# Kernel tuning notes

Measured on AMD Instinct MI355X. Metric: run time of the kernel, lower is better.

## Reference

```python
import jax, jax.numpy as jnp
import numpy as np

DIM = 192; HEADS = 6; WIN = 8; HIDDEN = int(DIM * 2.66); EPS = 1e-5

def dct_matrix(n):
    # DCT-II orthonormal matrix, matches get_dctMatrix(n, n)
    i = np.arange(n)[:, None]; j = np.arange(n)[None, :]
    M = np.cos(np.pi * i * (2 * j + 1) / (2 * n)) * np.sqrt(2.0 / n)
    M[0, :] = np.sqrt(1.0 / n)
    return jnp.asarray(M, dtype=jnp.float32)

def layernorm_c(x, w, b):
    # WithBias LayerNorm over channel dim of BCHW (restormer to_3d/to_4d style)
    mu = x.mean(axis=1, keepdims=True)
    var = ((x - mu) ** 2).mean(axis=1, keepdims=True)
    return (x - mu) / jnp.sqrt(var + EPS) * w[None, :, None, None] + b[None, :, None, None]

def conv1x1(x, w, b=None):
    y = jnp.einsum('oc,bchw->bohw', w, x)
    return y if b is None else y + b[None, :, None, None]

def dwconv3x3(x, w):
    return jax.lax.conv_general_dilated(x, w, (1, 1), ((1, 1), (1, 1)),
        dimension_numbers=('NCHW', 'OIHW', 'NCHW'), feature_group_count=x.shape[1])

def l2norm(x):
    n = jnp.sqrt(jnp.sum(x * x, axis=-1, keepdims=True))
    return x / jnp.maximum(n, 1e-12)

def window_channel_attn(qkv, temperature):
    # 'b (z head c) (h1 h) (w1 w) -> z (b h1 w1) head c (h w)'
    b, _, H, W = qkv.shape
    cph = DIM // HEADS
    h1, w1 = H // WIN, W // WIN
    t = qkv.reshape(b, 3, HEADS, cph, h1, WIN, w1, WIN)
    t = t.transpose(1, 0, 4, 6, 2, 3, 5, 7).reshape(3, b * h1 * w1, HEADS, cph, WIN * WIN)
    q, k, v = t[0], t[1], t[2]
    q = l2norm(q); k = l2norm(k)
    attn = jnp.einsum('nhce,nhde->nhcd', q, k) * temperature[None]  # channel x channel per window
    attn = jax.nn.softmax(attn, axis=-1)
    out = jnp.einsum('nhcd,nhde->nhce', attn, v)
    out = out.reshape(b, h1, w1, HEADS, cph, WIN, WIN)
    out = out.transpose(0, 3, 4, 1, 5, 2, 6).reshape(b, DIM, H, W)
    return out

def forward(x, norm1_w, norm1_b, w_qkv, w_dw, temperature, w_proj, b_proj,
            norm2_w, norm2_b, w_in, w_dwf, w_out):
    B, C, H, W = x.shape
    Mh = dct_matrix(H); Mw = dct_matrix(W)
    # attention branch in DCT domain
    y = layernorm_c(x, norm1_w, norm1_b)
    y = jnp.einsum('ph,bchw->bcpw', Mh, y)      # dct2dx: Mh @ y @ Mw.T
    y = jnp.einsum('bcpw,qw->bcpq', y, Mw)
    qkv = dwconv3x3(conv1x1(y, w_qkv), w_dw)
    a = window_channel_attn(qkv, temperature)
    a = conv1x1(a, w_proj, b_proj)
    a = jnp.einsum('bcpq,qw->bcpw', a, Mw)      # idct2dx: Mh.T @ a @ Mw
    a = jnp.einsum('bcpw,ph->bchw', a, Mh)
    x1 = x + a
    # gated-dconv FFN branch
    z = layernorm_c(x1, norm2_w, norm2_b)
    f = dwconv3x3(conv1x1(z, w_in), w_dwf)
    f1, f2 = jnp.split(f, 2, axis=1)
    f = jax.nn.gelu(f1, approximate=False) * f2
    f = conv1x1(f, w_out)
    return x1 + f

def setup_inputs() -> dict:
    key = jax.random.key(0)
    ks = jax.random.split(key, 8)
    B, C, H, W = 2, DIM, 192, 192
    s = 0.02
    return {
        'x': jax.random.normal(ks[0], (B, C, H, W), jnp.float32),
        'norm1_w': jnp.ones((C,), jnp.float32),
        'norm1_b': jnp.zeros((C,), jnp.float32),
        'w_qkv': jax.random.normal(ks[1], (3 * C, C), jnp.float32) * s,
        'w_dw': jax.random.normal(ks[2], (3 * C, 1, 3, 3), jnp.float32) * s,
        'temperature': jnp.ones((HEADS, 1, 1), jnp.float32) / np.float32(np.sqrt(C)),
        'w_proj': jax.random.normal(ks[3], (C, C), jnp.float32) * s,
        'b_proj': jnp.zeros((C,), jnp.float32),
        'norm2_w': jnp.ones((C,), jnp.float32),
        'norm2_b': jnp.zeros((C,), jnp.float32),
        'w_in': jax.random.normal(ks[4], (2 * HIDDEN, C), jnp.float32) * s,
        'w_dwf': jax.random.normal(ks[5], (2 * HIDDEN, 1, 3, 3), jnp.float32) * s,
        'w_out': jax.random.normal(ks[6], (C, HIDDEN), jnp.float32) * s,
    }

def reference(x, norm1_w, norm1_b, w_qkv, w_dw, temperature, w_proj, b_proj,
              norm2_w, norm2_b, w_in, w_dwf, w_out):
    return forward(x, norm1_w, norm1_b, w_qkv, w_dw, temperature, w_proj, b_proj,
                   norm2_w, norm2_b, w_in, w_dwf, w_out)
```

## Files before the change

### kernel.cpp

```cpp
#include <hip/hip_runtime.h>
#include <hip/hip_bf16.h>

typedef __hip_bfloat16 bft;
typedef __attribute__((ext_vector_type(8))) short bf16x8;
typedef __attribute__((ext_vector_type(4))) float f32x4;

#define BLK 256
static constexpr int Cc = 192;
static constexpr int L  = 192;
static constexpr int S  = 36864;
static constexpr int Bn = 2;
static constexpr int HID = 510;
static constexpr int CH2 = 96;
static constexpr int FTR2 = (CH2 + 2) * L;
static constexpr int GTR2 = CH2 * L;
static constexpr int DWS = 225;
static constexpr double PI_D = 3.141592653589793238462643383279502884;

__device__ __forceinline__ float ldf(const float* p) { return *p; }
__device__ __forceinline__ float ldf(const bft* p)   { return __bfloat162float(*p); }
__device__ __forceinline__ void  stf(float* p, float v) { *p = v; }
__device__ __forceinline__ void  stf(bft* p, float v)   { *p = __float2bfloat16(v); }
__device__ __forceinline__ unsigned short f2bfu(float f) {
    bft h = __float2bfloat16(f);
    return *reinterpret_cast<const unsigned short*>(&h);
}
__device__ __forceinline__ float bu2f(unsigned short u) {
    unsigned int x = (unsigned int)u << 16;
    return __uint_as_float(x);
}
__device__ __forceinline__ bf16x8 ld8(const unsigned short* p) {
    union { unsigned int u[4]; bf16x8 v; } t;
    const unsigned int* q = reinterpret_cast<const unsigned int*>(p);
    t.u[0] = q[0]; t.u[1] = q[1]; t.u[2] = q[2]; t.u[3] = q[3];
    return t.v;
}
__device__ __forceinline__ void softbar() {
    asm volatile("s_waitcnt lgkmcnt(0)" ::: "memory");
    __builtin_amdgcn_sched_barrier(0);
    __builtin_amdgcn_s_barrier();
}

__global__ __launch_bounds__(BLK) void k_dct_init(bft* __restrict__ dctb,
                                                  bft* __restrict__ dctTb) {
    int idx = blockIdx.x * BLK + threadIdx.x;
    if (idx >= L * L) return;
    int p = idx / L, h = idx - p * L;
    double v = (p == 0) ? sqrt(1.0 / L)
                        : cos(PI_D * p * (2 * h + 1) / (2.0 * L)) * sqrt(2.0 / L);
    bft bv = __float2bfloat16((float)v);
    dctb[p * L + h] = bv;
    dctTb[h * L + p] = bv;
}

__global__ __launch_bounds__(BLK) void k_cvt(const float* __restrict__ src,
                                             bft* __restrict__ dst,
                                             int Mr, int Kr, int Kp) {
    int idx = blockIdx.x * BLK + threadIdx.x;
    int m = idx / Kp, k = idx - m * Kp;
    float v = (m < Mr && k < Kr) ? src[(size_t)m * Kr + k] : 0.f;
    dst[idx] = __float2bfloat16(v);
}

__global__ __launch_bounds__(BLK) void k_cvt_ffn(const float* __restrict__ src,
                                                 bft* __restrict__ dst) {
    int idx = blockIdx.x * BLK + threadIdx.x;
    int m = idx / Cc, k = idx - m * Cc;
    float v = 0.f;
    if (m < 510) v = src[(size_t)m * Cc + k];
    else if (m >= 512 && m < 1022) v = src[(size_t)(m - 2) * Cc + k];
    dst[idx] = __float2bfloat16(v);
}

template <typename TI, bool TRANS>
__global__ __launch_bounds__(BLK) void k_lnt(const TI* __restrict__ x,
                                             const float* __restrict__ w,
                                             const float* __restrict__ b,
                                             bft* __restrict__ out,
                                             long zI, long zO) {
    __shared__ float t[192][65];
    __shared__ float mus[64], rs[64];
    const int tid = threadIdx.x;
    const int s0 = blockIdx.x * 64;
    const TI* xp = x + (size_t)blockIdx.y * zI;
    if constexpr (sizeof(TI) == 4) {
        for (int id = tid; id < 192 * 16; id += BLK) {
            int c = id >> 4, q = id & 15;
            float4 v = *reinterpret_cast<const float4*>(
                (const float*)xp + (size_t)c * S + s0 + q * 4);
            t[c][q * 4 + 0] = v.x; t[c][q * 4 + 1] = v.y;
            t[c][q * 4 + 2] = v.z; t[c][q * 4 + 3] = v.w;
        }
    } else {
        for (int id = tid; id < 192 * 8; id += BLK) {
            int c = id >> 3, q = id & 7;
            uint4 raw = *reinterpret_cast<const uint4*>(
                (const bft*)xp + (size_t)c * S + s0 + q * 8);
            const unsigned short* u = reinterpret_cast<const unsigned short*>(&raw);
#pragma unroll
            for (int e = 0; e < 8; ++e) t[c][q * 8 + e] = bu2f(u[e]);
        }
    }
    __syncthreads();
    {
        int px = tid >> 2, g = tid & 3;
        float sum = 0.f, sq = 0.f;
#pragma unroll
        for (int j = 0; j < 48; ++j) {
            float v = t[g * 48 + j][px];
            sum += v; sq += v * v;
        }
        sum += __shfl_xor(sum, 1); sum += __shfl_xor(sum, 2);
        sq  += __shfl_xor(sq, 1);  sq  += __shfl_xor(sq, 2);
        float mu = sum * (1.f / Cc);
        float var = sq * (1.f / Cc) - mu * mu;
        float r = rsqrtf(var + 1e-5f);
        if (g == 0) { mus[px] = mu; rs[px] = r; }
    }
    __syncthreads();
    bft* op = out + (size_t)blockIdx.y * zO;
    if constexpr (!TRANS) {
        for (int id = tid; id < 192 * 8; id += BLK) {
            int c = id >> 3, q = id & 7;
            float wc = w[c], bc = b[c];
            unsigned short v8[8];
#pragma unroll
            for (int e = 0; e < 8; ++e) {
                int px = q * 8 + e;
                v8[e] = f2bfu((t[c][px] - mus[px]) * rs[px] * wc + bc);
            }
            *reinterpret_cast<uint4*>(op + (size_t)c * S + s0 + q * 8) =
                *reinterpret_cast<uint4*>(v8);
        }
    } else {
#pragma unroll
        for (int qq = 0; qq < 3; ++qq) {
            for (int id = tid; id < 512; id += BLK) {
                int s = id >> 3, qlo = id & 7;
                int q = qq * 8 + qlo;
                float mu = mus[s], r = rs[s];
                unsigned short v8[8];
#pragma unroll
                for (int e = 0; e < 8; ++e) {
                    int c = q * 8 + e;
                    v8[e] = f2bfu((t[c][s] - mu) * r * w[c] + b[c]);
                }
                *reinterpret_cast<uint4*>(op + (size_t)(s0 + s) * Cc + q * 8) =
                    *reinterpret_cast<uint4*>(v8);
            }
        }
    }
}

__global__ __launch_bounds__(BLK) void k_tr(const bft* __restrict__ in,
                                            bft* __restrict__ out, long z) {
    __shared__ unsigned short t[32][72];
    const int tid = threadIdx.x;
    const int s0 = blockIdx.x * 64, c0 = blockIdx.y * 32;
    const bft* ip = in + (size_t)blockIdx.z * z;
    bft* op = out + (size_t)blockIdx.z * z;
    {
        int c = tid >> 3, sc = (tid & 7) * 8;
        *reinterpret_cast<uint4*>(&t[c][sc]) =
            *reinterpret_cast<const uint4*>(ip + (size_t)(c0 + c) * S + s0 + sc);
    }
    __syncthreads();
    {
        int s = tid >> 2, cc = (tid & 3) * 8;
        unsigned short v[8];
#pragma unroll
        for (int q = 0; q < 8; ++q) v[q] = t[cc + q][s];
        *reinterpret_cast<uint4*>(op + (size_t)(s0 + s) * Cc + c0 + cc) =
            *reinterpret_cast<uint4*>(v);
    }
}

__global__ __launch_bounds__(BLK) void k_w2s(const bft* __restrict__ src,
                                             bft* __restrict__ dst,
                                             long zI, long zO) {
    __shared__ unsigned short t[192][100];
    const int tid = threadIdx.x;
    const int hh = blockIdx.x;
    const int ch0 = blockIdx.y * 96;
    const int bz = blockIdx.z;
    const int h1 = hh >> 3, ii = hh & 7;
    const bft* ip = src + (size_t)bz * zI;
    for (int id = tid; id < 192 * 12; id += BLK) {
        int r = id / 12, q = id - r * 12;
        int w1 = r >> 3, jj = r & 7;
        int s = (h1 * 24 + w1) * 64 + ii * 8 + jj;
        *reinterpret_cast<uint4*>(&t[r][q * 8]) =
            *reinterpret_cast<const uint4*>(ip + (size_t)s * Cc + ch0 + q * 8);
    }
    __syncthreads();
    bft* op = dst + (size_t)bz * zO;
    for (int id = tid; id < 96 * 24; id += BLK) {
        int c = id / 24, q = id - c * 24;
        unsigned short v[8];
#pragma unroll
        for (int e = 0; e < 8; ++e) v[e] = t[q * 8 + e][c];
        *reinterpret_cast<uint4*>(op + (size_t)(ch0 + c) * S + (size_t)hh * L + q * 8) =
            *reinterpret_cast<uint4*>(v);
    }
}

template <int WR, int WC, int FM, int FN, int KSTEP, int BMODE, int OMODE,
          bool GSWAP, bool SWIZ, bool AMASK, bool HASBIAS, bool BIASN,
          bool HASRES, typename OutT, typename ResT>
__global__ __launch_bounds__(256) void k_mm(
    const bft* __restrict__ A, int strideA, int Mreal, long zA,
    const bft* __restrict__ B, int strideB, long zB,
    OutT* __restrict__ Out, int strideO, long zO,
    const float* __restrict__ bias,
    const ResT* __restrict__ Res, long zR,
    int K, int rlo, int rhi) {
    static_assert(WR == 2 && WC == 2, "split epilogues assume 2x2 waves");
    constexpr int BM = WR * FM * 16, BN = WC * FN * 16;
    constexpr int AV = KSTEP / 8;
    constexpr int KL = (BM + BN) * (KSTEP + 8);
    constexpr int RSTH = (OMODE == 3) ? (BN / 2) * (BM + 8)
                       : (OMODE == 5 ? (BM / 2) * (BN + 8) : 0);
    constexpr int LDSZ = (KL > RSTH) ? KL : RSTH;
    __shared__ unsigned short lds[LDSZ];
    unsigned short (*Al)[KSTEP + 8] =
        reinterpret_cast<unsigned short(*)[KSTEP + 8]>(lds);
    unsigned short (*Bl)[KSTEP + 8] =
        reinterpret_cast<unsigned short(*)[KSTEP + 8]>(lds + BM * (KSTEP + 8));
    const int tid = threadIdx.x;
    int bx = blockIdx.x, by = blockIdx.y;
    if constexpr (SWIZ) {
        int nbx = gridDim.x, nby = gridDim.y;
        int nwg = nbx * nby;
        int orig = bx + nbx * by;
        int cpx = nwg >> 3;
        int swz = (orig & 7) * cpx + (orig >> 3);
        bx = swz % nbx; by = swz / nbx;
    }
    const int n0 = (GSWAP ? by : bx) * BN;
    const int m0 = (GSWAP ? bx : by) * BM;
    const int bz = blockIdx.z;
    const int lane = tid & 63, wv = tid >> 6;
    const int wr = wv / WC, wc = wv % WC;
    const int l15 = lane & 15, l4 = lane >> 4;
    f32x4 acc[FM][FN] = {};

    const bft* Ab = A + (size_t)bz * zA;
    const bft* Bb = B + (size_t)bz * zB;

    for (int k0 = 0; k0 < K; k0 += KSTEP) {
        for (int id = tid; id < BM * AV; id += 256) {
            int row = id / AV, kc = (id % AV) * 8;
            int gm = m0 + row;
            if constexpr (AMASK) {
                uint4 val = make_uint4(0, 0, 0, 0);
                if (gm >= rlo && gm < rhi)
                    val = *reinterpret_cast<const uint4*>(
                        Ab + (size_t)gm * strideA + k0 + kc);
                *reinterpret_cast<uint4*>(&Al[row][kc]) = val;
            } else {
                if (gm >= Mreal) gm = Mreal - 1;
                *reinterpret_cast<uint4*>(&Al[row][kc]) =
                    *reinterpret_cast<const uint4*>(Ab + (size_t)gm * strideA + k0 + kc);
            }
        }
        for (int id = tid; id < BN * AV; id += 256) {
            int row = id / AV, kc = (id % AV) * 8;
            int gn = n0 + row;
            uint4 val;
            if constexpr (BMODE == 2) {
                val = *reinterpret_cast<const uint4*>(
                    Bb + (size_t)gn * strideB + k0 + kc);
            } else {
                if (gn >= rlo && gn < rhi)
                    val = *reinterpret_cast<const uint4*>(
                        Bb + (size_t)gn * strideB + k0 + kc);
                else
                    val = make_uint4(0, 0, 0, 0);
            }
            *reinterpret_cast<uint4*>(&Bl[row][kc]) = val;
        }
        __syncthreads();
#pragma unroll
        for (int kk = 0; kk < KSTEP / 32; ++kk) {
            bf16x8 af[FM], bf[FN];
#pragma unroll
            for (int i = 0; i < FM; ++i)
                af[i] = *reinterpret_cast<const bf16x8*>(
                    &Al[wr * FM * 16 + i * 16 + l15][kk * 32 + l4 * 8]);
#pragma unroll
            for (int j = 0; j < FN; ++j)
                bf[j] = *reinterpret_cast<const bf16x8*>(
                    &Bl[wc * FN * 16 + j * 16 + l15][kk * 32 + l4 * 8]);
#pragma unroll
            for (int i = 0; i < FM; ++i)
#pragma unroll
                for (int j = 0; j < FN; ++j)
                    acc[i][j] = __builtin_amdgcn_mfma_f32_16x16x32_bf16(
                        af[i], bf[j], acc[i][j], 0, 0, 0);
        }
        __syncthreads();
    }
    if constexpr (OMODE == 3) {
        constexpr int OST = BM + 8;
        constexpr int HBN = BN / 2;
        unsigned short* Ol = lds;
        constexpr int TPR = BM / 64;
#pragma unroll
        for (int h = 0; h < 2; ++h) {
            if (wc == h) {
#pragma unroll
                for (int i = 0; i < FM; ++i) {
                    int mB = wr * FM * 16 + i * 16 + l4 * 4;
#pragma unroll
                    for (int j = 0; j < FN; ++j) {
                        int nl = j * 16 + l15;
                        unsigned short v[4];
#pragma unroll
                        for (int r = 0; r < 4; ++r) v[r] = f2bfu(acc[i][j][r]);
                        *reinterpret_cast<uint2*>(&Ol[nl * OST + mB]) =
                            *reinterpret_cast<uint2*>(v);
                    }
                }
            }
            softbar();
            for (int row = tid / TPR; row < HBN; row += 256 / TPR) {
                int seg = (tid % TPR) * 64;
                bft* dst = (bft*)Out + (size_t)bz * zO
                         + (size_t)(n0 + h * HBN + row) * strideO + m0 + seg;
                const unsigned short* src = &Ol[row * OST + seg];
#pragma unroll
                for (int q = 0; q < 8; ++q)
                    *reinterpret_cast<uint4*>(dst + q * 8) =
                        *reinterpret_cast<const uint4*>(src + q * 8);
            }
            if (h == 0) softbar();
        }
        return;
    }
    if constexpr (OMODE == 5) {
        constexpr int OST = BN + 8;
        constexpr int HBM = BM / 2;
        unsigned short* Ol = lds;
        constexpr int TPR = BN / 64;
#pragma unroll
        for (int h = 0; h < 2; ++h) {
            if (wr == h) {
#pragma unroll
                for (int i = 0; i < FM; ++i) {
                    int mBl = i * 16 + l4 * 4;
#pragma unroll
                    for (int j = 0; j < FN; ++j) {
                        int n = wc * FN * 16 + j * 16 + l15;
                        float bn = 0.f;
                        if constexpr (HASBIAS && BIASN) bn = bias[n0 + n];
#pragma unroll
                        for (int r = 0; r < 4; ++r)
                            Ol[(mBl + r) * OST + n] = f2bfu(acc[i][j][r] + bn);
                    }
                }
            }
            softbar();
            for (int row = tid / TPR; row < HBM; row += 256 / TPR) {
                int m = m0 + h * HBM + row;
                if (m >= Mreal) continue;
                int seg = (tid % TPR) * 64;
                bft* dst = (bft*)Out + (size_t)bz * zO
                         + (size_t)m * strideO + n0 + seg;
                const unsigned short* src = &Ol[row * OST + seg];
                if constexpr (HASRES) {
                    const ResT* res = Res + (size_t)bz * zR
                                    + (size_t)m * strideO + n0 + seg;
#pragma unroll
                    for (int q = 0; q < 8; ++q) {
                        uint4 lv = *reinterpret_cast<const uint4*>(src + q * 8);
                        const unsigned short* le =
                            reinterpret_cast<const unsigned short*>(&lv);
                        unsigned short ov[8];
#pragma unroll
                        for (int e = 0; e < 8; ++e)
                            ov[e] = f2bfu(bu2f(le[e]) + ldf(res + q * 8 + e));
                        *reinterpret_cast<uint4*>(dst + q * 8) =
                            *reinterpret_cast<uint4*>(ov);
                    }
                } else {
#pragma unroll
                    for (int q = 0; q < 8; ++q)
                        *reinterpret_cast<uint4*>(dst + q * 8) =
                            *reinterpret_cast<const uint4*>(src + q * 8);
                }
            }
            if (h == 0) softbar();
        }
        return;
    }
#pragma unroll
    for (int i = 0; i < FM; ++i) {
        int mB = m0 + wr * FM * 16 + i * 16 + l4 * 4;
#pragma unroll
        for (int j = 0; j < FN; ++j) {
            int n = n0 + wc * FN * 16 + j * 16 + l15;
#pragma unroll
            for (int r = 0; r < 4; ++r) {
                int m = mB + r;
                if (m >= Mreal) continue;
                float vv = acc[i][j][r];
                if constexpr (HASBIAS) vv += BIASN ? bias[n] : bias[m];
                size_t idx = (size_t)bz * zO + (size_t)m * strideO + n;
                if constexpr (HASRES)
                    vv += ldf(Res + (size_t)bz * zR + (size_t)m * strideO + n);
                stf(Out + idx, vv);
            }
        }
    }
}

__global__ __launch_bounds__(BLK) void k_dwconv3b(const bft* __restrict__ qkv,
                                                  const float* __restrict__ wt,
                                                  bft* __restrict__ q_out,
                                                  bft* __restrict__ k_out,
                                                  bft* __restrict__ v_out,
                                                  long CSl) {
    __shared__ float t[10 * DWS];
    const int tid = threadIdx.x;
    const int ch3 = blockIdx.x;
    const int wr = blockIdx.y;
    const int b = ch3 / 576, zc = ch3 - b * 576;
    const int z = zc / Cc, ch = zc - z * Cc;
    const int h0 = wr * 8;
    const bft* ip = qkv + (size_t)b * 3 * CSl + (size_t)zc * S;
    for (int id = tid; id < 240; id += BLK) {
        int row = id / 24, q = id - row * 24;
        int gh = h0 - 1 + row;
        float e[8];
        if (gh >= 0 && gh < L) {
            uint4 raw = *reinterpret_cast<const uint4*>(ip + (size_t)gh * L + q * 8);
            const unsigned short* u = reinterpret_cast<const unsigned short*>(&raw);
#pragma unroll
            for (int ee = 0; ee < 8; ++ee) e[ee] = bu2f(u[ee]);
        } else {
#pragma unroll
            for (int ee = 0; ee < 8; ++ee) e[ee] = 0.f;
        }
#pragma unroll
        for (int ee = 0; ee < 8; ++ee) t[row * DWS + 1 + q * 8 + ee] = e[ee];
    }
    if (tid < 10) { t[tid * DWS] = 0.f; t[tid * DWS + 193] = 0.f; }
    __syncthreads();
    if (tid >= 192) return;
    float wv9[9];
#pragma unroll
    for (int i = 0; i < 9; ++i) wv9[i] = wt[(size_t)zc * 9 + i];
    const int wl = tid >> 3;
    const int ii = tid & 7;
    const int w0 = wl * 8;
    float acc[8] = {};
#pragma unroll
    for (int dy = 0; dy < 3; ++dy) {
        const float* rowp = &t[(ii + dy) * DWS + w0];
#pragma unroll
        for (int dx = 0; dx < 3; ++dx) {
            float wgt = wv9[dy * 3 + dx];
#pragma unroll
            for (int jj = 0; jj < 8; ++jj)
                acc[jj] += wgt * rowp[jj + dx];
        }
    }
    bft* base = (z == 0) ? q_out : (z == 1) ? k_out : v_out;
    unsigned short ov[8];
#pragma unroll
    for (int jj = 0; jj < 8; ++jj) ov[jj] = f2bfu(acc[jj]);
    *reinterpret_cast<uint4*>(base + (size_t)b * CSl + (size_t)ch * S
                              + (size_t)(wr * 24 + wl) * 64 + ii * 8) =
        *reinterpret_cast<uint4*>(ov);
}

__global__ __launch_bounds__(256) void k_attn_mfma(
    const bft* __restrict__ QW, long zQ,
    const bft* __restrict__ KW, long zK,
    const bft* __restrict__ VW, long zV,
    const float* __restrict__ temp,
    bft* __restrict__ outp, long zO) {
    __shared__ unsigned short qls[4][32 * 66];
    __shared__ unsigned short kls[4][32 * 66];
    __shared__ unsigned short vls[4][32 * 66];
    __shared__ float rqs[4][32], rks[4][32];
    const int tid = threadIdx.x;
    const int wv = tid >> 6, lane = tid & 63;
    const int win = blockIdx.x * 4 + wv;
    const int hd = blockIdx.y;
    const int bz = blockIdx.z;
    const int l15 = lane & 15, l4 = lane >> 4;
    unsigned short* ql = qls[wv];
    unsigned short* kl = kls[wv];
    unsigned short* vl = vls[wv];
    const size_t base = (size_t)(hd * 32) * S + (size_t)win * 64;

#pragma unroll
    for (int i = 0; i < 4; ++i) {
        int c = i * 8 + (lane >> 3), e0 = (lane & 7) * 8;
        size_t g = base + (size_t)c * S + e0;
        uint4 vq = *reinterpret_cast<const uint4*>(QW + (size_t)bz * zQ + g);
        uint4 vk = *reinterpret_cast<const uint4*>(KW + (size_t)bz * zK + g);
        uint4 vvv = *reinterpret_cast<const uint4*>(VW + (size_t)bz * zV + g);
        unsigned int* dq = reinterpret_cast<unsigned int*>(&ql[c * 66 + e0]);
        unsigned int* dk = reinterpret_cast<unsigned int*>(&kl[c * 66 + e0]);
        unsigned int* dv = reinterpret_cast<unsigned int*>(&vl[c * 66 + e0]);
        dq[0] = vq.x; dq[1] = vq.y; dq[2] = vq.z; dq[3] = vq.w;
        dk[0] = vk.x; dk[1] = vk.y; dk[2] = vk.z; dk[3] = vk.w;
        dv[0] = vvv.x; dv[1] = vvv.y; dv[2] = vvv.z; dv[3] = vvv.w;
    }
    __syncthreads();
    {
        int row = lane & 31;
        const unsigned short* src = (lane < 32) ? ql : kl;
        float s = 0.f;
#pragma unroll
        for (int w = 0; w < 32; ++w) {
            unsigned int d = *reinterpret_cast<const unsigned int*>(&src[row * 66 + 2 * w]);
            float a = bu2f((unsigned short)(d & 0xffff));
            float b = bu2f((unsigned short)(d >> 16));
            s += a * a + b * b;
        }
        float r = 1.f / fmaxf(sqrtf(s), 1e-12f);
        if (lane < 32) rqs[wv][row] = r; else rks[wv][row] = r;
    }
    __syncthreads();
    f32x4 at[2][2] = {};
#pragma unroll
    for (int ks = 0; ks < 2; ++ks) {
        bf16x8 aq[2], bk[2];
#pragma unroll
        for (int i = 0; i < 2; ++i)
            aq[i] = ld8(&ql[(i * 16 + l15) * 66 + ks * 32 + l4 * 8]);
#pragma unroll
        for (int j = 0; j < 2; ++j)
            bk[j] = ld8(&kl[(j * 16 + l15) * 66 + ks * 32 + l4 * 8]);
#pragma unroll
        for (int i = 0; i < 2; ++i)
#pragma unroll
            for (int j = 0; j < 2; ++j)
                at[i][j] = __builtin_amdgcn_mfma_f32_16x16x32_bf16(
                    aq[i], bk[j], at[i][j], 0, 0, 0);
    }
    float tpr = temp[hd];
    float rk0 = rks[wv][l15] * tpr, rk1 = rks[wv][16 + l15] * tpr;
    float pr[2][2][4];
#pragma unroll
    for (int i = 0; i < 2; ++i)
#pragma unroll
        for (int r = 0; r < 4; ++r) {
            int c = i * 16 + l4 * 4 + r;
            float rq = rqs[wv][c];
            float v0 = at[i][0][r] * rq * rk0;
            float v1 = at[i][1][r] * rq * rk1;
            float mx = fmaxf(v0, v1);
#pragma unroll
            for (int m = 1; m < 16; m <<= 1) mx = fmaxf(mx, __shfl_xor(mx, m));
            v0 = __expf(v0 - mx);
            v1 = __expf(v1 - mx);
            float sm = v0 + v1;
#pragma unroll
            for (int m = 1; m < 16; m <<= 1) sm += __shfl_xor(sm, m);
            float inv = 1.f / sm;
            pr[i][0][r] = v0 * inv;
            pr[i][1][r] = v1 * inv;
        }
    __syncthreads();
    unsigned short* pl = ql;
#pragma unroll
    for (int i = 0; i < 2; ++i)
#pragma unroll
        for (int j = 0; j < 2; ++j)
#pragma unroll
            for (int r = 0; r < 4; ++r)
                pl[(i * 16 + l4 * 4 + r) * 34 + j * 16 + l15] = f2bfu(pr[i][j][r]);
    __syncthreads();
    bf16x8 ap[2];
#pragma unroll
    for (int i = 0; i < 2; ++i)
        ap[i] = ld8(&pl[(i * 16 + l15) * 34 + l4 * 8]);
    f32x4 o[2][4] = {};
#pragma unroll
    for (int j = 0; j < 4; ++j) {
        unsigned short tv[8];
#pragma unroll
        for (int q = 0; q < 8; ++q)
            tv[q] = vl[(l4 * 8 + q) * 66 + j * 16 + l15];
        bf16x8 bv = *reinterpret_cast<bf16x8*>(tv);
#pragma unroll
        for (int i = 0; i < 2; ++i)
            o[i][j] = __builtin_amdgcn_mfma_f32_16x16x32_bf16(ap[i], bv, o[i][j], 0, 0, 0);
    }
#pragma unroll
    for (int i = 0; i < 2; ++i)
#pragma unroll
        for (int j = 0; j < 4; ++j) {
            int e = j * 16 + l15, cl = i * 16 + l4 * 4;
            unsigned short v[4];
#pragma unroll
            for (int r = 0; r < 4; ++r) v[r] = f2bfu(o[i][j][r]);
            unsigned short* row = ((e < 32) ? kl : vl) + (e & 31) * 40 + cl;
            *reinterpret_cast<uint2*>(row) = *reinterpret_cast<uint2*>(v);
        }
    {
        const unsigned short* row = ((lane < 32) ? kl : vl) + (lane & 31) * 40;
        bft* dst = outp + (size_t)bz * zO + (size_t)(win * 64 + lane) * Cc + hd * 32;
#pragma unroll
        for (int q = 0; q < 4; ++q)
            *reinterpret_cast<uint4*>(dst + q * 8) =
                *reinterpret_cast<const uint4*>(row + q * 8);
    }
}

__global__ __launch_bounds__(BLK) void k_gateT(const bft* __restrict__ fTg,
                                               const float* __restrict__ wt,
                                               bft* __restrict__ gTg) {
    __shared__ float w1s[64][9];
    __shared__ float w2s[64][9];
    const int tid = threadIdx.x;
    const int cbase = blockIdx.y * 64;
    const bft* fT = fTg + (size_t)blockIdx.z * FTR2 * 1024;
    bft* gT = gTg + (size_t)blockIdx.z * GTR2 * 512;
    for (int id = tid; id < 576; id += BLK) {
        int cl = id / 9, k = id - cl * 9;
        int c = cbase + cl;
        w1s[cl][k] = (c < HID) ? wt[(size_t)c * 9 + k] : 0.f;
        w2s[cl][k] = (c < HID) ? wt[(size_t)(c + HID) * 9 + k] : 0.f;
    }
    __syncthreads();
    int px = blockIdx.x * 32 + (tid >> 3);
    int cgl = (tid & 7) * 8;
    int hc = px / L, w = px - hc * L;
    float a1[8] = {}, a2[8] = {};
#pragma unroll
    for (int dy = 0; dy < 3; ++dy) {
#pragma unroll
        for (int dx = 0; dx < 3; ++dx) {
            int ww = w + dx - 1;
            if (ww < 0 || ww >= L) continue;
            size_t frow = (size_t)((hc + dy) * L + ww) * 1024 + cbase + cgl;
            uint4 u1 = *reinterpret_cast<const uint4*>(fT + frow);
            uint4 u2 = *reinterpret_cast<const uint4*>(fT + frow + 512);
            const unsigned short* e1 = reinterpret_cast<const unsigned short*>(&u1);
            const unsigned short* e2 = reinterpret_cast<const unsigned short*>(&u2);
            int k = dy * 3 + dx;
#pragma unroll
            for (int j = 0; j < 8; ++j) {
                a1[j] += w1s[cgl + j][k] * bu2f(e1[j]);
                a2[j] += w2s[cgl + j][k] * bu2f(e2[j]);
            }
        }
    }
    unsigned short ov[8];
#pragma unroll
    for (int j = 0; j < 8; ++j) {
        float ge = 0.5f * a1[j] * (1.f + erff(a1[j] * 0.70710678118654752f));
        ov[j] = f2bfu(ge * a2[j]);
    }
    *reinterpret_cast<uint4*>(gT + (size_t)px * 512 + cbase + cgl) =
        *reinterpret_cast<uint4*>(ov);
}

extern "C" void kernel_launch(void* const* d_in, const int* in_sizes, int n_in,
                              void* d_out, int out_size, void* d_ws, size_t ws_size,
                              hipStream_t stream) {
    const float* x      = (const float*)d_in[0];
    const float* n1w    = (const float*)d_in[1];
    const float* n1b    = (const float*)d_in[2];
    const float* w_qkv  = (const float*)d_in[3];
    const float* w_dw   = (const float*)d_in[4];
    const float* temp   = (const float*)d_in[5];
    const float* w_proj = (const float*)d_in[6];
    const float* b_proj = (const float*)d_in[7];
    const float* n2w    = (const float*)d_in[8];
    const float* n2b    = (const float*)d_in[9];
    const float* w_in   = (const float*)d_in[10];
    const float* w_dwf  = (const float*)d_in[11];
    const float* w_out  = (const float*)d_in[12];
    float* outp = (float*)d_out;

    const long CS = (long)Cc * S;
    const size_t DCT_B = 147456;
    const size_t BUF_B = (size_t)Bn * CS * 2;
    const size_t QKV_B = (size_t)Bn * 3 * CS * 2;
    const size_t WB_B  = 884736;
    const size_t GT_B  = (size_t)Bn * GTR2 * 512 * 2;
    const size_t NEED  = DCT_B + 4 * BUF_B + QKV_B + WB_B + GT_B;
    if (ws_size < NEED) return;

    char* p = (char*)d_ws;
    bft* dctb  = (bft*)p;
    bft* dctTb = dctb + L * L;
    p += DCT_B;
    bft* X1    = (bft*)p;                  p += BUF_B;
    bft* PbB   = (bft*)p;                  p += BUF_B;
    bft* QbB   = (bft*)p;                  p += BUF_B;
    bft* VW    = (bft*)p;                  p += BUF_B;
    bft* QKV   = (bft*)p;                  p += QKV_B;
    bft* w_qkv_b = (bft*)p;
    bft* w_proj_b = w_qkv_b + 576 * 192;
    bft* w_in_b  = w_proj_b + 192 * 192;
    bft* w_out_b = w_in_b + 1024 * 192;
    p += WB_B;
    bft* gT = (bft*)p;
    bft* fT = QKV;
    bft* attnT = QKV + CS;

    k_dct_init<<<144, BLK, 0, stream>>>(dctb, dctTb);
    k_cvt<<<432, BLK, 0, stream>>>(w_qkv, w_qkv_b, 576, 192, 192);
    k_cvt<<<144, BLK, 0, stream>>>(w_proj, w_proj_b, 192, 192, 192);
    k_cvt_ffn<<<768, BLK, 0, stream>>>(w_in, w_in_b);
    k_cvt<<<384, BLK, 0, stream>>>(w_out, w_out_b, 192, 510, 512);

    k_lnt<float, false><<<dim3(S / 64, Bn), BLK, 0, stream>>>(x, n1w, n1b, PbB, CS, CS);
    k_mm<2, 2, 2, 6, 32, 2, 3, false, false, false, false, false, false, bft, float><<<dim3(1, 3, Bn * Cc), 256, 0, stream>>>(
        PbB, L, L, S,  dctb, L, 0,  QbB, L, S,  nullptr, nullptr, 0,  L, 0, 0);
    k_mm<2, 2, 2, 6, 32, 2, 3, false, false, false, false, false, false, bft, float><<<dim3(1, 3, Bn * Cc), 256, 0, stream>>>(
        QbB, L, L, S,  dctb, L, 0,  PbB, L, S,  nullptr, nullptr, 0,  L, 0, 0);
    k_tr<<<dim3(576, 6, Bn), BLK, 0, stream>>>(PbB, QbB, CS);
    k_mm<2, 2, 4, 4, 32, 2, 5, true, true, false, false, false, false, bft, float><<<dim3(5, 288, Bn), 256, 0, stream>>>(
        w_qkv_b, Cc, 576, 0,  QbB, Cc, CS,  QKV, S, 3 * CS,  nullptr, nullptr, 0,  Cc, 0, 0);
    k_dwconv3b<<<dim3(Bn * 576, 24), BLK, 0, stream>>>(QKV, w_dw, PbB, QbB, VW, CS);
    k_attn_mfma<<<dim3(144, 6, Bn), 256, 0, stream>>>(
        PbB, CS, QbB, CS, VW, CS, temp, attnT, 3 * CS);
    k_mm<2, 2, 2, 6, 32, 2, 5, false, false, false, true, true, false, bft, float><<<dim3(1, 576, Bn), 256, 0, stream>>>(
        attnT, Cc, S, 3 * CS,  w_proj_b, Cc, 0,  PbB, Cc, CS,  b_proj, (const float*)nullptr, 0,  Cc, 0, 0);
    k_w2s<<<dim3(192, 2, Bn), BLK, 0, stream>>>(PbB, QbB, CS, CS);
    k_mm<2, 2, 2, 6, 32, 2, 3, false, false, false, false, false, false, bft, float><<<dim3(1, 3, Bn * Cc), 256, 0, stream>>>(
        QbB, L, L, S,  dctTb, L, 0,  PbB, L, S,  nullptr, nullptr, 0,  L, 0, 0);
    k_mm<2, 2, 2, 6, 32, 2, 5, false, false, false, false, false, true, bft, float><<<dim3(1, 3, Bn * Cc), 256, 0, stream>>>(
        dctTb, L, L, 0,  PbB, L, S,  X1, L, S,  nullptr, x, S,  L, 0, 0);

    k_lnt<bft, true><<<dim3(S / 64, Bn), BLK, 0, stream>>>(X1, n2w, n2b, QbB, CS, CS);
    for (int ck = 0; ck < 2; ++ck) {
        int h0 = ck * CH2;
        long off = (long)(h0 - 1) * L;
        int rlo = (ck == 0) ? L : 0;
        int rhi = (ck == 1) ? (FTR2 - L) : FTR2;
        k_mm<2, 2, 4, 4, 32, 4, 3, true, true, false, false, false, false, bft, float><<<dim3(8, 147, Bn), 256, 0, stream>>>(
            w_in_b, Cc, 1024, 0,  QbB + off * Cc, Cc, CS,  fT, 1024, (long)FTR2 * 1024,
            nullptr, nullptr, 0,  Cc, rlo, rhi);
        k_gateT<<<dim3(GTR2 / 32, 8, Bn), BLK, 0, stream>>>(fT, w_dwf, gT);
        k_mm<2, 2, 2, 4, 32, 2, 0, true, true, false, false, false, true, float, bft><<<dim3(3, 144, Bn), 256, 0, stream>>>(
            w_out_b, 512, 192, 0,  gT, 512, (long)GTR2 * 512,
            outp + (size_t)ck * GTR2, S, CS,
            nullptr, X1 + (size_t)ck * GTR2, CS,  512, 0, 0);
    }
}
```

Baseline: 628.5 us.

## Prefetch next K-tile into registers while computing current tile in GEMM

The GEMM main loop now loads the next K-step's A and B tiles from global memory into registers before running the MFMA loop on the current LDS tile, then writes them to LDS on the next iteration. This software-pipelines the global load latency behind the matrix math. It costs extra registers per thread, which may lower occupancy. It also relies on BM*AV and BN*AV being multiples of 256 and on an existing softbar barrier helper.

```diff
diff --git a/kernel.cpp b/kernel.cpp
--- a/kernel.cpp
+++ b/kernel.cpp
@@ -217,6 +217,8 @@
     static_assert(WR == 2 && WC == 2, "split epilogues assume 2x2 waves");
     constexpr int BM = WR * FM * 16, BN = WC * FN * 16;
     constexpr int AV = KSTEP / 8;
+    constexpr int APT = BM * AV / 256;
+    constexpr int BPT = BN * AV / 256;
     constexpr int KL = (BM + BN) * (KSTEP + 8);
     constexpr int RSTH = (OMODE == 3) ? (BN / 2) * (BM + 8)
                        : (OMODE == 5 ? (BM / 2) * (BN + 8) : 0);
@@ -247,8 +249,11 @@
     const bft* Ab = A + (size_t)bz * zA;
     const bft* Bb = B + (size_t)bz * zB;
 
-    for (int k0 = 0; k0 < K; k0 += KSTEP) {
-        for (int id = tid; id < BM * AV; id += 256) {
+    uint4 pra[APT], prb[BPT];
+    auto loadA = [&](int k0) {
+#pragma unroll
+        for (int t = 0; t < APT; ++t) {
+            int id = tid + t * 256;
             int row = id / AV, kc = (id % AV) * 8;
             int gm = m0 + row;
             if constexpr (AMASK) {
@@ -256,30 +261,49 @@
                 if (gm >= rlo && gm < rhi)
                     val = *reinterpret_cast<const uint4*>(
                         Ab + (size_t)gm * strideA + k0 + kc);
-                *reinterpret_cast<uint4*>(&Al[row][kc]) = val;
+                pra[t] = val;
             } else {
                 if (gm >= Mreal) gm = Mreal - 1;
-                *reinterpret_cast<uint4*>(&Al[row][kc]) =
-                    *reinterpret_cast<const uint4*>(Ab + (size_t)gm * strideA + k0 + kc);
-            }
-        }
-        for (int id = tid; id < BN * AV; id += 256) {
+                pra[t] = *reinterpret_cast<const uint4*>(
+                    Ab + (size_t)gm * strideA + k0 + kc);
+            }
+        }
+    };
+    auto loadB = [&](int k0) {
+#pragma unroll
+        for (int t = 0; t < BPT; ++t) {
+            int id = tid + t * 256;
             int row = id / AV, kc = (id % AV) * 8;
             int gn = n0 + row;
-            uint4 val;
             if constexpr (BMODE == 2) {
-                val = *reinterpret_cast<const uint4*>(
+                prb[t] = *reinterpret_cast<const uint4*>(
                     Bb + (size_t)gn * strideB + k0 + kc);
             } else {
+                uint4 val = make_uint4(0, 0, 0, 0);
                 if (gn >= rlo && gn < rhi)
                     val = *reinterpret_cast<const uint4*>(
                         Bb + (size_t)gn * strideB + k0 + kc);
-                else
-                    val = make_uint4(0, 0, 0, 0);
-            }
-            *reinterpret_cast<uint4*>(&Bl[row][kc]) = val;
-        }
-        __syncthreads();
+                prb[t] = val;
+            }
+        }
+    };
+
+    loadA(0); loadB(0);
+    for (int k0 = 0; k0 < K; k0 += KSTEP) {
+#pragma unroll
+        for (int t = 0; t < APT; ++t) {
+            int id = tid + t * 256;
+            int row = id / AV, kc = (id % AV) * 8;
+            *reinterpret_cast<uint4*>(&Al[row][kc]) = pra[t];
+        }
+#pragma unroll
+        for (int t = 0; t < BPT; ++t) {
+            int id = tid + t * 256;
+            int row = id / AV, kc = (id % AV) * 8;
+            *reinterpret_cast<uint4*>(&Bl[row][kc]) = prb[t];
+        }
+        softbar();
+        if (k0 + KSTEP < K) { loadA(k0 + KSTEP); loadB(k0 + KSTEP); }
 #pragma unroll
         for (int kk = 0; kk < KSTEP / 32; ++kk) {
             bf16x8 af[FM], bf[FN];
@@ -298,7 +322,7 @@
                     acc[i][j] = __builtin_amdgcn_mfma_f32_16x16x32_bf16(
                         af[i], bf[j], acc[i][j], 0, 0, 0);
         }
-        __syncthreads();
+        softbar();
     }
     if constexpr (OMODE == 3) {
         constexpr int OST = BM + 8;
```

Measured after the change: 771.8 us. 22.8% more time.
